# Kernel tuning notes

Hardware: AMD Instinct MI355X
Metric: run time of the kernel (lower is better)

Reference implementation:

```python
import jax, jax.numpy as jnp
import numpy as np

B = 2048          # batch
D = 256           # agent input dim
S = 32            # num_splines
CANVAS = 128      # canvas_size
NUM_T = 50        # samples along each Bezier curve (hard-coded in module)
BRUSH = 1         # brush_size (hard-coded)
SCALE = 1e-4      # Normal scale hard-coded in forward (log_std is unused)
W_STAMP = -0.07   # per-stamp weight (hard-coded)
BG = 0.3          # background_shade


def setup_inputs() -> dict:
    key = jax.random.key(0)
    k1, k2 = jax.random.split(key, 2)
    x = jax.random.normal(k1, (B, D), dtype=jnp.float32)
    W_agent = jax.random.normal(k2, (D, S * 6), dtype=jnp.float32) * 0.05
    b_agent = jnp.zeros((S * 6,), dtype=jnp.float32)
    return {"x": x, "W_agent": W_agent, "b_agent": b_agent}


def _paint_multiple_splines(sample):
    # sample: [B, S*6] in (0,1)
    bsz = sample.shape[0]
    params = sample.reshape(bsz, -1, 6) * CANVAS          # [B, S, 6]
    P0 = params[..., 0:2][:, :, None, :]                   # [B, S, 1, 2]
    P1 = params[..., 2:4][:, :, None, :]
    P2 = params[..., 4:6][:, :, None, :]
    t = jnp.linspace(0.0, 1.0, NUM_T, dtype=params.dtype).reshape(1, 1, NUM_T, 1)
    # quadratic Bezier: [B, S, T, 2]
    spline_points = (1 - t) ** 2 * P0 + 2 * (1 - t) * t * P1 + t ** 2 * P2
    coords = jnp.round(spline_points).astype(jnp.int32)
    r = jnp.arange(-BRUSH, BRUSH + 1)
    dx, dy = jnp.meshgrid(r, r, indexing="ij")
    dx, dy = dx.ravel(), dy.ravel()                        # [9]
    x_idx = jnp.clip(coords[..., 0][..., None] + dx, 0, CANVAS - 1)  # [B,S,T,9]
    y_idx = jnp.clip(coords[..., 1][..., None] + dy, 0, CANVAS - 1)
    flat_idx = (x_idx * CANVAS + y_idx).reshape(bsz, -1)   # [B, S*T*9]
    weights = jnp.full(flat_idx.shape, W_STAMP, dtype=jnp.float32)
    canvas_flat = jnp.zeros((bsz, CANVAS * CANVAS), dtype=jnp.float32)
    canvas_flat = canvas_flat.at[jnp.arange(bsz)[:, None], flat_idx].add(weights)
    canvas = canvas_flat.reshape(bsz, CANVAS, CANVAS)
    return jnp.clip(canvas + BG, 0.0, 1.0)


def reference(x, W_agent, b_agent):
    mu = x @ W_agent + b_agent                             # [B, S*6]
    scale = jnp.float32(SCALE)
    log2pi = jnp.log(jnp.float32(2.0) * jnp.pi)
    dim = mu.shape[-1]
    # eval-time path: raw_sample = mu
    raw = mu
    log_prob = jnp.sum(
        -0.5 * ((raw - mu) / scale) ** 2 - jnp.log(scale) - 0.5 * log2pi,
        axis=-1,
    )                                                      # [B]
    entropy = jnp.full(
        (mu.shape[0],), dim * (0.5 + 0.5 * log2pi + jnp.log(scale)),
        dtype=jnp.float32,
    )                                                      # [B]
    sample = jax.nn.sigmoid(raw)                           # [B, S*6]
    sketch = _paint_multiple_splines(sample)               # [B, CANVAS, CANVAS]
    return sketch, log_prob, entropy, sample
```

## Files before the change

kernel.cpp:

```cpp
#include <hip/hip_runtime.h>
#include <math.h>

#define NB      2048
#define DIM     256
#define SC6     192
#define CV      128
#define NT      50

#define LPV  (1591.9491530441301f)
#define ENV  (-1495.9491530441301f)

#define SKETCH_N   ((size_t)NB * CV * CV)
#define LP_OFF     (SKETCH_N)
#define ENT_OFF    (LP_OFF + NB)
#define SAMPLE_OFF (ENT_OFF + NB)

__global__ __launch_bounds__(192) void gemm_sig_kernel(
    const float* __restrict__ x, const float* __restrict__ W,
    const float* __restrict__ bias, float* __restrict__ out,
    double* __restrict__ params)
{
    __shared__ float xt[DIM * 8];
    const int b0  = blockIdx.x * 8;
    const int tid = threadIdx.x;

    for (int idx = tid; idx < DIM * 8; idx += 192) {
        int i = idx >> 8;
        int d = idx & 255;
        xt[d * 8 + i] = x[(size_t)(b0 + i) * DIM + d];
    }
    __syncthreads();

    const int j = tid;
    double acc[8] = {0, 0, 0, 0, 0, 0, 0, 0};

    #pragma unroll 4
    for (int d = 0; d < DIM; ++d) {
        double wd = (double)W[d * SC6 + j];
        const float4* xp = (const float4*)(&xt[d * 8]);
        float4 xa = xp[0];
        float4 xb = xp[1];
        acc[0] = fma((double)xa.x, wd, acc[0]);
        acc[1] = fma((double)xa.y, wd, acc[1]);
        acc[2] = fma((double)xa.z, wd, acc[2]);
        acc[3] = fma((double)xa.w, wd, acc[3]);
        acc[4] = fma((double)xb.x, wd, acc[4]);
        acc[5] = fma((double)xb.y, wd, acc[5]);
        acc[6] = fma((double)xb.z, wd, acc[6]);
        acc[7] = fma((double)xb.w, wd, acc[7]);
    }

    const double bj = (double)bias[j];
    float* out_sample = out + SAMPLE_OFF;

    #pragma unroll
    for (int i = 0; i < 8; ++i) {
        double mu = acc[i] + bj;
        double s  = 1.0 / (1.0 + exp(-mu));
        out_sample[(size_t)(b0 + i) * SC6 + j] = (float)s;
        params[(size_t)(b0 + i) * SC6 + j]     = s * 128.0;
    }

    if (j < 8) {
        out[LP_OFF  + b0 + j] = LPV;
        out[ENT_OFF + b0 + j] = ENV;
    }
}

__global__ __launch_bounds__(256) void paint_kernel(
    const double* __restrict__ params, float* __restrict__ out)
{
    __shared__ unsigned int cnt[CV * CV / 2];
    __shared__ double sp[SC6];

    const int b   = blockIdx.x;
    const int tid = threadIdx.x;

    for (int w = tid; w < CV * CV / 2; w += 256) cnt[w] = 0u;
    if (tid < SC6) sp[tid] = params[(size_t)b * SC6 + tid];
    __syncthreads();

    for (int i = tid; i < 32 * NT; i += 256) {
        int s = i / NT;
        int k = i - s * NT;
        double t = (k == NT - 1) ? 1.0 : (double)k * (1.0 / 49.0);
        double u = 1.0 - t;
        double a  = u * u;
        double bq = (2.0 * u) * t;
        double c  = t * t;
        const double* P = &sp[s * 6];
        double px = a * P[0] + bq * P[2] + c * P[4];
        double py = a * P[1] + bq * P[3] + c * P[5];
        int cx = (int)rint(px);
        int cy = (int)rint(py);
        #pragma unroll
        for (int dx = -1; dx <= 1; ++dx) {
            #pragma unroll
            for (int dy = -1; dy <= 1; ++dy) {
                int xi = min(max(cx + dx, 0), CV - 1);
                int yi = min(max(cy + dy, 0), CV - 1);
                int p  = xi * CV + yi;
                atomicAdd(&cnt[p >> 1], 1u << ((p & 1) << 4));
            }
        }
    }
    __syncthreads();

    float4* ob = (float4*)(out + (size_t)b * CV * CV);
    const uint2* c2 = (const uint2*)cnt;
    for (int w = tid; w < CV * CV / 8; w += 256) {
        uint2 v = c2[w];
        unsigned int c0 = v.x & 0xFFFFu;
        unsigned int c1 = v.x >> 16;
        unsigned int c2v = v.y & 0xFFFFu;
        unsigned int c3 = v.y >> 16;
        double r0 = 0.3 - 0.07 * (double)c0;
        double r1 = 0.3 - 0.07 * (double)c1;
        double r2 = 0.3 - 0.07 * (double)c2v;
        double r3 = 0.3 - 0.07 * (double)c3;
        float4 r;
        r.x = (float)(r0 < 0.0 ? 0.0 : (r0 > 1.0 ? 1.0 : r0));
        r.y = (float)(r1 < 0.0 ? 0.0 : (r1 > 1.0 ? 1.0 : r1));
        r.z = (float)(r2 < 0.0 ? 0.0 : (r2 > 1.0 ? 1.0 : r2));
        r.w = (float)(r3 < 0.0 ? 0.0 : (r3 > 1.0 ? 1.0 : r3));
        ob[w] = r;
    }
}

extern "C" void kernel_launch(void* const* d_in, const int* in_sizes, int n_in,
                              void* d_out, int out_size, void* d_ws, size_t ws_size,
                              hipStream_t stream) {
    const float* x    = (const float*)d_in[0];
    const float* W    = (const float*)d_in[1];
    const float* bias = (const float*)d_in[2];
    float* out = (float*)d_out;
    double* params = (double*)d_ws;

    gemm_sig_kernel<<<NB / 8, 192, 0, stream>>>(x, W, bias, out, params);
    paint_kernel<<<NB, 256, 0, stream>>>(params, out);
}
```

Measured before the change: 195.1 us.

## Fuse GEMM+sigmoid into paint kernel and coalesce brush atomics with swizzled canvas

Merges the GEMM/sigmoid kernel into the per-batch paint kernel, so each block computes its 192 spline parameters from one row of x. This removes the workspace round-trip and one kernel launch. The 3x3 stamp is changed to pack the column increments of each row into one or two atomics on 16-bit-pair words, and the shared canvas is swizzled per row to spread LDS bank conflicts. Point indexing is reordered so that adjacent threads handle different splines. In exchange, each block rereads the whole W matrix, and the per-row matvec uses fp64 FMAs on only 192 threads with no reuse of W across batch rows.

New measurement: 168.2 us. 1.16x faster.

```diff
diff --git a/kernel.cpp b/kernel.cpp
--- a/kernel.cpp
+++ b/kernel.cpp
@@ -15,74 +15,45 @@
 #define ENT_OFF    (LP_OFF + NB)
 #define SAMPLE_OFF (ENT_OFF + NB)
 
-__global__ __launch_bounds__(192) void gemm_sig_kernel(
+__global__ __launch_bounds__(256) void fused_kernel(
     const float* __restrict__ x, const float* __restrict__ W,
-    const float* __restrict__ bias, float* __restrict__ out,
-    double* __restrict__ params)
-{
-    __shared__ float xt[DIM * 8];
-    const int b0  = blockIdx.x * 8;
-    const int tid = threadIdx.x;
-
-    for (int idx = tid; idx < DIM * 8; idx += 192) {
-        int i = idx >> 8;
-        int d = idx & 255;
-        xt[d * 8 + i] = x[(size_t)(b0 + i) * DIM + d];
-    }
-    __syncthreads();
-
-    const int j = tid;
-    double acc[8] = {0, 0, 0, 0, 0, 0, 0, 0};
-
-    #pragma unroll 4
-    for (int d = 0; d < DIM; ++d) {
-        double wd = (double)W[d * SC6 + j];
-        const float4* xp = (const float4*)(&xt[d * 8]);
-        float4 xa = xp[0];
-        float4 xb = xp[1];
-        acc[0] = fma((double)xa.x, wd, acc[0]);
-        acc[1] = fma((double)xa.y, wd, acc[1]);
-        acc[2] = fma((double)xa.z, wd, acc[2]);
-        acc[3] = fma((double)xa.w, wd, acc[3]);
-        acc[4] = fma((double)xb.x, wd, acc[4]);
-        acc[5] = fma((double)xb.y, wd, acc[5]);
-        acc[6] = fma((double)xb.z, wd, acc[6]);
-        acc[7] = fma((double)xb.w, wd, acc[7]);
-    }
-
-    const double bj = (double)bias[j];
-    float* out_sample = out + SAMPLE_OFF;
-
-    #pragma unroll
-    for (int i = 0; i < 8; ++i) {
-        double mu = acc[i] + bj;
-        double s  = 1.0 / (1.0 + exp(-mu));
-        out_sample[(size_t)(b0 + i) * SC6 + j] = (float)s;
-        params[(size_t)(b0 + i) * SC6 + j]     = s * 128.0;
-    }
-
-    if (j < 8) {
-        out[LP_OFF  + b0 + j] = LPV;
-        out[ENT_OFF + b0 + j] = ENV;
-    }
-}
-
-__global__ __launch_bounds__(256) void paint_kernel(
-    const double* __restrict__ params, float* __restrict__ out)
+    const float* __restrict__ bias, float* __restrict__ out)
 {
     __shared__ unsigned int cnt[CV * CV / 2];
     __shared__ double sp[SC6];
+    __shared__ float  xs[DIM];
 
     const int b   = blockIdx.x;
     const int tid = threadIdx.x;
 
-    for (int w = tid; w < CV * CV / 2; w += 256) cnt[w] = 0u;
-    if (tid < SC6) sp[tid] = params[(size_t)b * SC6 + tid];
+    {
+        uint4* c4 = (uint4*)cnt;
+        uint4 z = make_uint4(0u, 0u, 0u, 0u);
+        #pragma unroll
+        for (int w = 0; w < 8; ++w) c4[tid + 256 * w] = z;
+    }
+    xs[tid] = x[(size_t)b * DIM + tid];
+    if (tid == 192) out[LP_OFF  + b] = LPV;
+    if (tid == 193) out[ENT_OFF + b] = ENV;
+    __syncthreads();
+
+    if (tid < SC6) {
+        const int j = tid;
+        double acc = 0.0;
+        #pragma unroll 8
+        for (int d = 0; d < DIM; ++d) {
+            acc = fma((double)xs[d], (double)W[d * SC6 + j], acc);
+        }
+        double mu = acc + (double)bias[j];
+        double s  = 1.0 / (1.0 + exp(-mu));
+        out[SAMPLE_OFF + (size_t)b * SC6 + j] = (float)s;
+        sp[j] = s * 128.0;
+    }
     __syncthreads();
 
     for (int i = tid; i < 32 * NT; i += 256) {
-        int s = i / NT;
-        int k = i - s * NT;
+        int s = i & 31;
+        int k = i >> 5;
         double t = (k == NT - 1) ? 1.0 : (double)k * (1.0 / 49.0);
         double u = 1.0 - t;
         double a  = u * u;
@@ -93,31 +64,48 @@
         double py = a * P[1] + bq * P[3] + c * P[5];
         int cx = (int)rint(px);
         int cy = (int)rint(py);
+
+        int y0 = min(max(cy - 1, 0), CV - 1);
+        int y1 = min(max(cy,     0), CV - 1);
+        int y2 = min(max(cy + 1, 0), CV - 1);
+        int cb = y0 >> 1;
+        unsigned incA = 1u << ((y0 & 1) << 4);
+        unsigned incB = 0u;
+        unsigned i1 = 1u << ((y1 & 1) << 4);
+        unsigned i2 = 1u << ((y2 & 1) << 4);
+        if ((y1 >> 1) == cb) incA += i1; else incB += i1;
+        if ((y2 >> 1) == cb) incA += i2; else incB += i2;
+
+        int x0 = min(max(cx - 1, 0), CV - 1);
+        int x1 = min(max(cx,     0), CV - 1);
+        int x2 = min(max(cx + 1, 0), CV - 1);
+        int rows[3] = {x0, x1, x2};
         #pragma unroll
-        for (int dx = -1; dx <= 1; ++dx) {
-            #pragma unroll
-            for (int dy = -1; dy <= 1; ++dy) {
-                int xi = min(max(cx + dx, 0), CV - 1);
-                int yi = min(max(cy + dy, 0), CV - 1);
-                int p  = xi * CV + yi;
-                atomicAdd(&cnt[p >> 1], 1u << ((p & 1) << 4));
-            }
+        for (int r = 0; r < 3; ++r) {
+            int xi = rows[r];
+            int base = xi << 6;
+            int sw = 3 * xi;
+            atomicAdd(&cnt[base + ((cb + sw) & 63)], incA);
+            if (incB) atomicAdd(&cnt[base + ((cb + 1 + sw) & 63)], incB);
         }
     }
     __syncthreads();
 
     float4* ob = (float4*)(out + (size_t)b * CV * CV);
-    const uint2* c2 = (const uint2*)cnt;
-    for (int w = tid; w < CV * CV / 8; w += 256) {
-        uint2 v = c2[w];
-        unsigned int c0 = v.x & 0xFFFFu;
-        unsigned int c1 = v.x >> 16;
-        unsigned int c2v = v.y & 0xFFFFu;
-        unsigned int c3 = v.y >> 16;
-        double r0 = 0.3 - 0.07 * (double)c0;
-        double r1 = 0.3 - 0.07 * (double)c1;
-        double r2 = 0.3 - 0.07 * (double)c2v;
-        double r3 = 0.3 - 0.07 * (double)c3;
+    for (int w = tid; w < CV * CV / 4; w += 256) {
+        int pb = w << 2;
+        int xi = pb >> 7;
+        int c0 = (pb >> 1) & 63;
+        int base = xi << 6;
+        int sw = 3 * xi;
+        unsigned v0 = cnt[base + ((c0 + sw) & 63)];
+        unsigned v1 = cnt[base + ((c0 + 1 + sw) & 63)];
+        unsigned k0 = v0 & 0xFFFFu, k1 = v0 >> 16;
+        unsigned k2 = v1 & 0xFFFFu, k3 = v1 >> 16;
+        double r0 = 0.3 - 0.07 * (double)k0;
+        double r1 = 0.3 - 0.07 * (double)k1;
+        double r2 = 0.3 - 0.07 * (double)k2;
+        double r3 = 0.3 - 0.07 * (double)k3;
         float4 r;
         r.x = (float)(r0 < 0.0 ? 0.0 : (r0 > 1.0 ? 1.0 : r0));
         r.y = (float)(r1 < 0.0 ? 0.0 : (r1 > 1.0 ? 1.0 : r1));
@@ -134,8 +122,6 @@
     const float* W    = (const float*)d_in[1];
     const float* bias = (const float*)d_in[2];
     float* out = (float*)d_out;
-    double* params = (double*)d_ws;
 
-    gemm_sig_kernel<<<NB / 8, 192, 0, stream>>>(x, W, bias, out, params);
-    paint_kernel<<<NB, 256, 0, stream>>>(params, out);
+    fused_kernel<<<NB, 256, 0, stream>>>(x, W, bias, out);
 }
```
